# Optimization experiments

Hardware: AMD Instinct MI355X
Metric: run time of the kernel (lower is better)

## Reference

```python
import jax, jax.numpy as jnp
import numpy as np
import math

B, S, D, H = 4, 2048, 1024, 16
DH = D // H
NEG = -1e10


def setup_inputs() -> dict:
    key = jax.random.key(0)
    k1, k2, k3 = jax.random.split(key, 3)
    x = jax.random.normal(k1, (B, S, D), dtype=jnp.float32)
    # torch nn.Linear weights have shape (out_features, in_features); y = x @ W.T + b
    w1 = jax.random.normal(k2, (3 * D, D), dtype=jnp.float32) * (1.0 / math.sqrt(D))
    b1 = jnp.zeros((3 * D,), dtype=jnp.float32)
    w2 = jax.random.normal(k3, (D, D), dtype=jnp.float32) * (1.0 / math.sqrt(D))
    b2 = jnp.zeros((D,), dtype=jnp.float32)
    return {"x": x, "w1": w1, "b1": b1, "w2": w2, "b2": b2}


def reference(x, w1, b1, w2, b2):
    b, s, d = x.shape
    h, dh = H, d // H
    qkv = x @ w1.T + b1                                  # [B,S,3D]
    q, k, v = jnp.split(qkv, 3, axis=-1)                 # each [B,S,D]
    def heads(t):
        return t.reshape(b, s, h, dh).transpose(0, 2, 1, 3)  # [B,H,S,dh]
    q, k, v = heads(q), heads(k), heads(v)
    # additive causal mask: (1 - tril) * -1e10, as in the original
    mask = (1.0 - jnp.tril(jnp.ones((s, s), dtype=x.dtype))) * NEG
    scores = jnp.einsum('bhqd,bhkd->bhqk', q, k) / math.sqrt(dh) + mask
    attn = jax.nn.softmax(scores, axis=-1)
    o = jnp.einsum('bhqk,bhkd->bhqd', attn, v)           # [B,H,S,dh]
    o = o.transpose(0, 2, 1, 3).reshape(b, s, d)         # [B,S,D]
    return o @ w2.T + b2
```

## Files before the change

### kernel.cpp

```cpp
#include <hip/hip_runtime.h>
#include <stdint.h>


typedef __bf16 bf16;
typedef __attribute__((ext_vector_type(4))) __bf16 bf16x4;
typedef __attribute__((ext_vector_type(8))) __bf16 bf16x8;
typedef __attribute__((ext_vector_type(4))) float f32x4;
typedef __attribute__((ext_vector_type(16))) float f32x16;

#define MFMA16(a, b, c) __builtin_amdgcn_mfma_f32_16x16x32_bf16((a), (b), (c), 0, 0, 0)
#define MFMA32(a, b, c) __builtin_amdgcn_mfma_f32_32x32x16_bf16((a), (b), (c), 0, 0, 0)

#if __has_builtin(__builtin_amdgcn_exp2f)
#define EXP2F(x) __builtin_amdgcn_exp2f(x)
#else
#define EXP2F(x) exp2f(x)
#endif

#define GLOAD_LDS16(gp, lp)                                                    \
  __builtin_amdgcn_global_load_lds(                                            \
      (__attribute__((address_space(1))) void*)(gp),                           \
      (__attribute__((address_space(3))) void*)(lp), 16, 0, 0)

#define SB   2048
#define D3   3072
#define DD   1024
#define QSCALE 0.18033688011112042f

__global__ __launch_bounds__(256) void cast3_kernel(
    const float* __restrict__ x, const float* __restrict__ w1,
    const float* __restrict__ w2, bf16* __restrict__ xb,
    bf16* __restrict__ w1b, bf16* __restrict__ w2b) {
  const int stride = gridDim.x * blockDim.x;
  const int gid = blockIdx.x * blockDim.x + threadIdx.x;
  auto cvt = [](const float* in, bf16* out, int i) {
    float4 v = ((const float4*)in)[i];
    bf16x4 p;
    p[0] = (bf16)v.x; p[1] = (bf16)v.y; p[2] = (bf16)v.z; p[3] = (bf16)v.w;
    *(bf16x4*)(out + (size_t)i * 4) = p;
  };
  for (int i = gid; i < 2097152; i += stride) cvt(x, xb, i);
  for (int i = gid; i < 786432; i += stride) cvt(w1, w1b, i);
  for (int i = gid; i < 262144; i += stride) cvt(w2, w2b, i);
}

template <int OUTMODE, int WM, int WN, int FM, int FN>
__global__ __launch_bounds__(512, 1) void gemmks_kernel(
    const bf16* __restrict__ A, const bf16* __restrict__ Bw,
    const float* __restrict__ bias, void* __restrict__ Cout,
    int M, int N, int K, int NBn) {
  constexpr int BM = WM * FM * 32, BN = WN * FN * 32;
  constexpr int NRA = BM / 64, NRB = BN / 64;
  __shared__ __attribute__((aligned(16))) bf16 As[2][BM * 64];
  __shared__ __attribute__((aligned(16))) bf16 Bs[2][BN * 64];
  const int tid = threadIdx.x;
  const int w = tid >> 6, l = tid & 63;
  const int lr = l & 31, lh = l >> 5;
  const int wm = w / WN, wn = w % WN;
  const int nwg = gridDim.x;
  const int sw = ((int)blockIdx.x % 8) * (nwg / 8) + (int)blockIdx.x / 8;
  const int bn = sw % NBn, bm = sw / NBn;
  const int m0 = bm * BM, n0 = bn * BN;
  const int NT = K >> 6;

  const int srow = l >> 3;
  const int scol = ((l & 7) ^ srow) << 3;

  auto stage = [&](int buf, int kt) {
#pragma unroll
    for (int j = 0; j < NRA; ++j) {
      const int rb = j * 64 + w * 8 + srow;
      GLOAD_LDS16(A + (size_t)(m0 + rb) * K + kt * 64 + scol,
                  (char*)&As[buf][0] + j * 8192 + w * 1024);
    }
#pragma unroll
    for (int j = 0; j < NRB; ++j) {
      const int rb = j * 64 + w * 8 + srow;
      GLOAD_LDS16(Bw + (size_t)(n0 + rb) * K + kt * 64 + scol,
                  (char*)&Bs[buf][0] + j * 8192 + w * 1024);
    }
  };

  f32x16 acc[FM][FN] = {};

  stage(0, 0);
  __syncthreads();

  for (int T = 0; T < NT; ++T) {
    const int buf = T & 1;
    if (T + 1 < NT) stage(buf ^ 1, T + 1);
#pragma unroll
    for (int ks = 0; ks < 4; ++ks) {
      bf16x8 aF[FM], bF[FN];
#pragma unroll
      for (int ti = 0; ti < FM; ++ti) {
        const int r = wm * (FM * 32) + ti * 32 + lr;
        aF[ti] = *(const bf16x8*)((const char*)&As[buf][0] + r * 128 +
                                  (((ks * 2 + lh) ^ (lr & 7)) << 4));
      }
#pragma unroll
      for (int tj = 0; tj < FN; ++tj) {
        const int r = wn * (FN * 32) + tj * 32 + lr;
        bF[tj] = *(const bf16x8*)((const char*)&Bs[buf][0] + r * 128 +
                                  (((ks * 2 + lh) ^ (lr & 7)) << 4));
      }
      __builtin_amdgcn_s_setprio(1);
#pragma unroll
      for (int ti = 0; ti < FM; ++ti)
#pragma unroll
        for (int tj = 0; tj < FN; ++tj)
          acc[ti][tj] = MFMA32(aF[ti], bF[tj], acc[ti][tj]);
      __builtin_amdgcn_s_setprio(0);
    }
    __syncthreads();
  }

#pragma unroll
  for (int ti = 0; ti < FM; ++ti) {
    const int r0 = m0 + wm * (FM * 32) + ti * 32 + 4 * lh;
#pragma unroll
    for (int tj = 0; tj < FN; ++tj) {
      const int col = n0 + wn * (FN * 32) + tj * 32 + lr;
      const float bv = bias[col];
#pragma unroll
      for (int e = 0; e < 16; ++e) {
        const int row = r0 + (e & 3) + 8 * (e >> 2);
        float v = acc[ti][tj][e] + bv;
        if (OUTMODE == 1) {
          if (col < DD) v *= QSCALE;
          ((bf16*)Cout)[(size_t)row * N + col] = (bf16)v;
        } else {
          ((float*)Cout)[(size_t)row * N + col] = v;
        }
      }
    }
  }
}

__global__ __launch_bounds__(256) void vtrans_kernel(
    const bf16* __restrict__ qkv, bf16* __restrict__ vT) {
  __shared__ __attribute__((aligned(16))) bf16 tt[64 * 72];
  const int tid = threadIdx.x;
  const int bh = blockIdx.x >> 5, st = blockIdx.x & 31;
  const int b = bh >> 4, h = bh & 15;
  const int s0 = st * 64;
  const int sr = tid >> 3, c0 = (tid & 7) * 8;
#pragma unroll
  for (int i = 0; i < 2; ++i) {
    const int srr = sr + i * 32;
    bf16x8 v = *(const bf16x8*)(qkv + (size_t)(b * SB + s0 + srr) * D3 + 2 * DD + h * 64 + c0);
    *(bf16x8*)(&tt[srr * 72 + c0]) = v;
  }
  __syncthreads();
  const int d = tid >> 2;
#pragma unroll
  for (int i = 0; i < 2; ++i) {
    const int sc = (tid & 3) * 2 + i;
    bf16x8 v;
#pragma unroll
    for (int j = 0; j < 8; ++j) v[j] = tt[(sc * 8 + j) * 72 + d];
    *(bf16x8*)(vT + (size_t)(bh * 64 + d) * SB + s0 + sc * 8) = v;
  }
}

__global__ __launch_bounds__(256, 2) void attn_kernel(
    const bf16* __restrict__ qkv, const bf16* __restrict__ vT,
    bf16* __restrict__ o) {
  __shared__ __attribute__((aligned(16))) bf16 Kt[2][128 * 64];
  __shared__ __attribute__((aligned(16))) bf16 Vt[2][64 * 128];
  const int tid = threadIdx.x;
  const int w = tid >> 6, l = tid & 63;
  const int c = l & 15, g = l >> 4;
  const int pair = blockIdx.x >> 6, bh = blockIdx.x & 63;
  const int b = bh >> 4, h = bh & 15;
  const int qtA = pair, qtB = 15 - pair;
  const int swz = (c & 7) << 4;

  const bf16* qg = qkv + (size_t)(b * SB) * D3 + h * 64;

  auto stage = [&](int kt, int buf) {
#pragma unroll
    for (int j = 0; j < 4; ++j) {
      const int row = w * 32 + j * 8 + (l >> 3);
      const int cs = ((l & 7) ^ (row & 7)) << 3;
      GLOAD_LDS16(qkv + (size_t)(b * SB + kt * 128 + row) * D3 + DD + h * 64 + cs,
                  (char*)&Kt[buf][0] + w * 4096 + j * 1024);
    }
#pragma unroll
    for (int j = 0; j < 4; ++j) {
      const int row = w * 16 + j * 4 + (l >> 4);
      const int cs = ((l & 15) ^ (row & 7)) << 3;
      GLOAD_LDS16(vT + (size_t)(bh * 64 + row) * SB + kt * 128 + cs,
                  (char*)&Vt[buf][0] + w * 4096 + j * 1024);
    }
  };

  stage(0, 0);

  bf16x8 qfA[2][2], qfB[2][2];
#pragma unroll
  for (int mi = 0; mi < 2; ++mi)
#pragma unroll
    for (int dk = 0; dk < 2; ++dk) {
      qfA[mi][dk] = *(const bf16x8*)(qg + (size_t)(qtA * 128 + w * 32 + mi * 16 + c) * D3 + dk * 32 + g * 8);
      qfB[mi][dk] = *(const bf16x8*)(qg + (size_t)(qtB * 128 + w * 32 + mi * 16 + c) * D3 + dk * 32 + g * 8);
    }

  f32x4 ofA[2][4] = {}, ofB[2][4] = {};
  float mA[2] = {-1e30f, -1e30f}, lA[2] = {0.f, 0.f};
  float mB[2] = {-1e30f, -1e30f}, lB[2] = {0.f, 0.f};
  const f32x4 zero = {0.f, 0.f, 0.f, 0.f};

  auto process = [&](int kt, int qt, int buf, bf16x8 (&qf)[2][2], float (&m)[2],
                     float (&lsum)[2], f32x4 (&of)[2][4]) {
    f32x4 sf[2][8];
    __builtin_amdgcn_s_setprio(1);
#pragma unroll
    for (int f = 0; f < 8; ++f) {
      const char* kr = (const char*)&Kt[buf][0] + (f * 16 + c) * 128;
      bf16x8 kb0 = *(const bf16x8*)(kr + ((g * 16) ^ swz));
      bf16x8 kb1 = *(const bf16x8*)(kr + ((64 + g * 16) ^ swz));
#pragma unroll
      for (int mi = 0; mi < 2; ++mi) {
        f32x4 t = MFMA16(kb0, qf[mi][0], zero);
        sf[mi][f] = MFMA16(kb1, qf[mi][1], t);
      }
    }
    __builtin_amdgcn_s_setprio(0);

    if (kt == qt) {
#pragma unroll
      for (int mi = 0; mi < 2; ++mi) {
        const int qloc = w * 32 + mi * 16 + c;
#pragma unroll
        for (int f = 0; f < 8; ++f)
#pragma unroll
          for (int r = 0; r < 4; ++r)
            if (f * 16 + 4 * g + r > qloc) sf[mi][f][r] = -1e30f;
      }
    }

    bf16x8 pa[2][4];
#pragma unroll
    for (int mi = 0; mi < 2; ++mi) {
      float pm = -1e30f;
#pragma unroll
      for (int f = 0; f < 8; ++f)
#pragma unroll
        for (int r = 0; r < 4; ++r) pm = fmaxf(pm, sf[mi][f][r]);
      pm = fmaxf(pm, __shfl_xor(pm, 16, 64));
      pm = fmaxf(pm, __shfl_xor(pm, 32, 64));
      if (__any(pm > m[mi] + 8.f)) {
        const float mnew = fmaxf(m[mi], pm);
        const float sc = EXP2F(m[mi] - mnew);
        m[mi] = mnew;
        lsum[mi] *= sc;
#pragma unroll
        for (int di = 0; di < 4; ++di) of[mi][di] *= sc;
      }
      float rs = 0.f;
#pragma unroll
      for (int f = 0; f < 8; ++f)
#pragma unroll
        for (int r = 0; r < 4; ++r) {
          const float pv = EXP2F(sf[mi][f][r] - m[mi]);
          sf[mi][f][r] = pv;
          rs += pv;
        }
      rs += __shfl_xor(rs, 16, 64);
      rs += __shfl_xor(rs, 32, 64);
      lsum[mi] += rs;
#pragma unroll
      for (int t = 0; t < 4; ++t)
#pragma unroll
        for (int s = 0; s < 4; ++s) {
          pa[mi][t][s]     = (bf16)sf[mi][2 * t][s];
          pa[mi][t][4 + s] = (bf16)sf[mi][2 * t + 1][s];
        }
    }

    __builtin_amdgcn_s_setprio(1);
#pragma unroll
    for (int di = 0; di < 4; ++di) {
      const char* vrow = (const char*)&Vt[buf][0] + (di * 16 + c) * 256;
#pragma unroll
      for (int t = 0; t < 4; ++t) {
        bf16x4 v1 = *(const bf16x4*)(vrow + ((64 * t + 8 * g) ^ swz));
        bf16x4 v2 = *(const bf16x4*)(vrow + ((64 * t + 32 + 8 * g) ^ swz));
        bf16x8 va;
#pragma unroll
        for (int s = 0; s < 4; ++s) { va[s] = v1[s]; va[4 + s] = v2[s]; }
#pragma unroll
        for (int mi = 0; mi < 2; ++mi)
          of[mi][di] = MFMA16(va, pa[mi][t], of[mi][di]);
      }
    }
    __builtin_amdgcn_s_setprio(0);
  };

  __syncthreads();

  int buf = 0;
  for (int kt = 0; kt <= qtB; ++kt) {
    if (kt < qtB) stage(kt + 1, buf ^ 1);
    if (kt <= qtA) process(kt, qtA, buf, qfA, mA, lA, ofA);
    process(kt, qtB, buf, qfB, mB, lB, ofB);
    __syncthreads();
    buf ^= 1;
  }

  auto store_tile = [&](int qt, float (&lsum)[2], f32x4 (&of)[2][4]) {
#pragma unroll
    for (int mi = 0; mi < 2; ++mi) {
      const float inv = 1.0f / lsum[mi];
      const size_t row = (size_t)(b * SB + qt * 128 + w * 32 + mi * 16 + c);
#pragma unroll
      for (int di = 0; di < 4; ++di) {
        bf16x4 st;
#pragma unroll
        for (int r = 0; r < 4; ++r) st[r] = (bf16)(of[mi][di][r] * inv);
        *(bf16x4*)(o + row * DD + h * 64 + di * 16 + 4 * g) = st;
      }
    }
  };
  store_tile(qtA, lA, ofA);
  store_tile(qtB, lB, ofB);
}

extern "C" void kernel_launch(void* const* d_in, const int* in_sizes, int n_in,
                              void* d_out, int out_size, void* d_ws, size_t ws_size,
                              hipStream_t stream) {
  const float* x  = (const float*)d_in[0];
  const float* w1 = (const float*)d_in[1];
  const float* b1 = (const float*)d_in[2];
  const float* w2 = (const float*)d_in[3];
  const float* b2 = (const float*)d_in[4];
  float* out = (float*)d_out;

  bf16* xb   = (bf16*)d_ws;
  bf16* w1b  = xb   + (size_t)8  * 1024 * 1024;
  bf16* w2b  = w1b  + (size_t)3  * 1024 * 1024;
  bf16* qkvb = w2b  + (size_t)1  * 1024 * 1024;
  bf16* vT   = qkvb + (size_t)8192 * 3072;
  bf16* ob   = vT   + (size_t)8  * 1024 * 1024;

  cast3_kernel<<<2048, 256, 0, stream>>>(x, w1, w2, xb, w1b, w2b);

  gemmks_kernel<1, 2, 4, 4, 3><<<256, 512, 0, stream>>>(xb, w1b, b1, qkvb, 8192, 3072, 1024, 8);
  vtrans_kernel<<<2048, 256, 0, stream>>>(qkvb, vT);
  attn_kernel<<<512, 256, 0, stream>>>(qkvb, vT, ob);
  gemmks_kernel<0, 4, 2, 2, 2><<<256, 512, 0, stream>>>(ob, w2b, b2, out, 8192, 1024, 1024, 8);
}
```

Measured before the change: 160.9 us.

## Replace big-tile GEMM with small 128x128x32 tiles at higher occupancy

```diff
diff --git a/kernel.cpp b/kernel.cpp
--- a/kernel.cpp
+++ b/kernel.cpp
@@ -44,44 +44,47 @@
   for (int i = gid; i < 262144; i += stride) cvt(w2, w2b, i);
 }
 
-template <int OUTMODE, int WM, int WN, int FM, int FN>
-__global__ __launch_bounds__(512, 1) void gemmks_kernel(
+template <int OUTMODE>
+__global__ __launch_bounds__(256, 4) void gemm97_kernel(
     const bf16* __restrict__ A, const bf16* __restrict__ Bw,
     const float* __restrict__ bias, void* __restrict__ Cout,
     int M, int N, int K, int NBn) {
-  constexpr int BM = WM * FM * 32, BN = WN * FN * 32;
-  constexpr int NRA = BM / 64, NRB = BN / 64;
-  __shared__ __attribute__((aligned(16))) bf16 As[2][BM * 64];
-  __shared__ __attribute__((aligned(16))) bf16 Bs[2][BN * 64];
+  __shared__ __attribute__((aligned(16))) bf16 As[2][128 * 32];
+  __shared__ __attribute__((aligned(16))) bf16 Bs[2][128 * 32];
   const int tid = threadIdx.x;
   const int w = tid >> 6, l = tid & 63;
   const int lr = l & 31, lh = l >> 5;
-  const int wm = w / WN, wn = w % WN;
+  const int wm = w >> 1, wn = w & 1;
   const int nwg = gridDim.x;
   const int sw = ((int)blockIdx.x % 8) * (nwg / 8) + (int)blockIdx.x / 8;
   const int bn = sw % NBn, bm = sw / NBn;
-  const int m0 = bm * BM, n0 = bn * BN;
-  const int NT = K >> 6;
-
-  const int srow = l >> 3;
-  const int scol = ((l & 7) ^ srow) << 3;
+  const int m0 = bm * 128, n0 = bn * 128;
+  const int NT = K >> 5;
 
   auto stage = [&](int buf, int kt) {
 #pragma unroll
-    for (int j = 0; j < NRA; ++j) {
-      const int rb = j * 64 + w * 8 + srow;
-      GLOAD_LDS16(A + (size_t)(m0 + rb) * K + kt * 64 + scol,
-                  (char*)&As[buf][0] + j * 8192 + w * 1024);
-    }
-#pragma unroll
-    for (int j = 0; j < NRB; ++j) {
-      const int rb = j * 64 + w * 8 + srow;
-      GLOAD_LDS16(Bw + (size_t)(n0 + rb) * K + kt * 64 + scol,
-                  (char*)&Bs[buf][0] + j * 8192 + w * 1024);
-    }
-  };
-
-  f32x16 acc[FM][FN] = {};
+    for (int j = 0; j < 2; ++j) {
+      const int row = j * 64 + w * 16 + (l >> 2);
+      const int s = ((l & 3) ^ (row & 3) ^ ((row >> 2) & 3)) << 3;
+      GLOAD_LDS16(A + (size_t)(m0 + row) * K + kt * 32 + s,
+                  (char*)&As[buf][0] + (j * 64 + w * 16) * 64);
+      GLOAD_LDS16(Bw + (size_t)(n0 + row) * K + kt * 32 + s,
+                  (char*)&Bs[buf][0] + (j * 64 + w * 16) * 64);
+    }
+  };
+
+  auto ldA = [&](int buf, int mi, int ks) -> bf16x8 {
+    const int r = wm * 64 + mi * 32 + lr;
+    const int ch = (ks * 2 + lh) ^ (r & 3) ^ ((r >> 2) & 3);
+    return *(const bf16x8*)((const char*)&As[buf][0] + r * 64 + ch * 16);
+  };
+  auto ldB = [&](int buf, int nj, int ks) -> bf16x8 {
+    const int r = wn * 64 + nj * 32 + lr;
+    const int ch = (ks * 2 + lh) ^ (r & 3) ^ ((r >> 2) & 3);
+    return *(const bf16x8*)((const char*)&Bs[buf][0] + r * 64 + ch * 16);
+  };
+
+  f32x16 acc[2][2] = {};
 
   stage(0, 0);
   __syncthreads();
@@ -90,37 +93,26 @@
     const int buf = T & 1;
     if (T + 1 < NT) stage(buf ^ 1, T + 1);
 #pragma unroll
-    for (int ks = 0; ks < 4; ++ks) {
-      bf16x8 aF[FM], bF[FN];
-#pragma unroll
-      for (int ti = 0; ti < FM; ++ti) {
-        const int r = wm * (FM * 32) + ti * 32 + lr;
-        aF[ti] = *(const bf16x8*)((const char*)&As[buf][0] + r * 128 +
-                                  (((ks * 2 + lh) ^ (lr & 7)) << 4));
-      }
-#pragma unroll
-      for (int tj = 0; tj < FN; ++tj) {
-        const int r = wn * (FN * 32) + tj * 32 + lr;
-        bF[tj] = *(const bf16x8*)((const char*)&Bs[buf][0] + r * 128 +
-                                  (((ks * 2 + lh) ^ (lr & 7)) << 4));
-      }
+    for (int ks = 0; ks < 2; ++ks) {
+      bf16x8 aF[2], bF[2];
+      aF[0] = ldA(buf, 0, ks); aF[1] = ldA(buf, 1, ks);
+      bF[0] = ldB(buf, 0, ks); bF[1] = ldB(buf, 1, ks);
       __builtin_amdgcn_s_setprio(1);
-#pragma unroll
-      for (int ti = 0; ti < FM; ++ti)
-#pragma unroll
-        for (int tj = 0; tj < FN; ++tj)
-          acc[ti][tj] = MFMA32(aF[ti], bF[tj], acc[ti][tj]);
+      acc[0][0] = MFMA32(aF[0], bF[0], acc[0][0]);
+      acc[0][1] = MFMA32(aF[0], bF[1], acc[0][1]);
+      acc[1][0] = MFMA32(aF[1], bF[0], acc[1][0]);
+      acc[1][1] = MFMA32(aF[1], bF[1], acc[1][1]);
       __builtin_amdgcn_s_setprio(0);
     }
     __syncthreads();
   }
 
 #pragma unroll
-  for (int ti = 0; ti < FM; ++ti) {
-    const int r0 = m0 + wm * (FM * 32) + ti * 32 + 4 * lh;
-#pragma unroll
-    for (int tj = 0; tj < FN; ++tj) {
-      const int col = n0 + wn * (FN * 32) + tj * 32 + lr;
+  for (int ti = 0; ti < 2; ++ti) {
+    const int r0 = m0 + wm * 64 + ti * 32 + 4 * lh;
+#pragma unroll
+    for (int tj = 0; tj < 2; ++tj) {
+      const int col = n0 + wn * 64 + tj * 32 + lr;
       const float bv = bias[col];
 #pragma unroll
       for (int e = 0; e < 16; ++e) {
@@ -346,8 +338,8 @@
 
   cast3_kernel<<<2048, 256, 0, stream>>>(x, w1, w2, xb, w1b, w2b);
 
-  gemmks_kernel<1, 2, 4, 4, 3><<<256, 512, 0, stream>>>(xb, w1b, b1, qkvb, 8192, 3072, 1024, 8);
+  gemm97_kernel<1><<<1536, 256, 0, stream>>>(xb, w1b, b1, qkvb, 8192, 3072, 1024, 24);
   vtrans_kernel<<<2048, 256, 0, stream>>>(qkvb, vT);
   attn_kernel<<<512, 256, 0, stream>>>(qkvb, vT, ob);
-  gemmks_kernel<0, 4, 2, 2, 2><<<256, 512, 0, stream>>>(ob, w2b, b2, out, 8192, 1024, 1024, 8);
-}
+  gemm97_kernel<0><<<512, 256, 0, stream>>>(ob, w2b, b2, out, 8192, 1024, 1024, 8);
+}
```

Result: slower. 177.1 us (+10.1%).
